# Performance work log

Hardware: AMD Instinct MI355X
Metric: run time of the kernel (lower is better)

Reference implementation:

```python
import jax, jax.numpy as jnp
import numpy as np

D_MODEL = 512
H = 8
DH = D_MODEL // H
P = H * (H - 1) // 2  # 28 head pairs
THRESH = 0.1
B, N = 2, 2048

# pair indices (i<j) in the same row-major order as the nested torch loop
_I_IDX, _J_IDX = np.triu_indices(H, k=1)
I_IDX = jnp.asarray(_I_IDX)
J_IDX = jnp.asarray(_J_IDX)


def setup_inputs() -> dict:
    key = jax.random.key(0)
    ks = jax.random.split(key, 10)
    s = 1.0 / np.sqrt(D_MODEL)
    return {
        "x": jax.random.normal(ks[0], (B, N, D_MODEL), dtype=jnp.float32),
        "Wq": jax.random.normal(ks[1], (D_MODEL, D_MODEL), dtype=jnp.float32) * s,
        "bq": jnp.zeros((D_MODEL,), dtype=jnp.float32),
        "Wk": jax.random.normal(ks[2], (D_MODEL, D_MODEL), dtype=jnp.float32) * s,
        "bk": jnp.zeros((D_MODEL,), dtype=jnp.float32),
        "Wv": jax.random.normal(ks[3], (D_MODEL, D_MODEL), dtype=jnp.float32) * s,
        "bv": jnp.zeros((D_MODEL,), dtype=jnp.float32),
        "Wo": jax.random.normal(ks[4], (D_MODEL, D_MODEL), dtype=jnp.float32) * s,
        "bo": jnp.zeros((D_MODEL,), dtype=jnp.float32),
        # stacked restriction maps: (P, DH_out, DH_in), Linear(bias=False)
        "Wr": jax.random.normal(ks[5], (P, DH, DH), dtype=jnp.float32) / np.sqrt(DH),
        "agreement_scale": jnp.asarray(1.0, dtype=jnp.float32),
    }


def reference(x, Wq, bq, Wk, bk, Wv, bv, Wo, bo, Wr, agreement_scale):
    b, n, d = x.shape
    # projections (torch Linear: y = x @ W.T + b), split into heads -> (B,H,N,DH)
    q = (x @ Wq.T + bq).reshape(b, n, H, DH).transpose(0, 2, 1, 3)
    k = (x @ Wk.T + bk).reshape(b, n, H, DH).transpose(0, 2, 1, 3)
    v = (x @ Wv.T + bv).reshape(b, n, H, DH).transpose(0, 2, 1, 3)

    scores = jnp.einsum("bhnd,bhmd->bhnm", q, k) / jnp.sqrt(jnp.asarray(DH, x.dtype))
    attn = jax.nn.softmax(scores, axis=-1)
    head_out = jnp.einsum("bhnm,bhmd->bhnd", attn, v)  # (B,H,N,DH)

    # --- pairwise restriction-map agreement, fully batched over the P pairs ---
    hi = head_out[:, I_IDX]  # (B,P,N,DH)
    hj = head_out[:, J_IDX]  # (B,P,N,DH)
    ri = jnp.einsum("bpnd,ped->bpne", hi, Wr)  # per-pair Linear(bias=False)
    diff = jnp.linalg.norm(ri - hj, axis=-1).mean(axis=-1)  # (B,P)
    score = jnp.exp(-diff * agreement_scale / THRESH)  # (B,P)

    agreement = jnp.zeros((b, H, H), dtype=x.dtype)
    agreement = agreement.at[:, I_IDX, J_IDX].set(score)
    agreement = agreement.at[:, J_IDX, I_IDX].set(score)
    diag = jnp.arange(H)
    agreement = agreement.at[:, diag, diag].set(1.0)

    # --- consensus aggregation ---
    offdiag = 1.0 - jnp.eye(H, dtype=x.dtype)
    consensus = (agreement * offdiag).sum(axis=-1) / (H - 1)  # (B,H)
    filtered = consensus * (consensus > THRESH).astype(x.dtype)
    weights = jax.nn.softmax(filtered + 1e-10, axis=-1)  # (B,H)

    agg = (head_out * weights[:, :, None, None]).sum(axis=1)  # (B,N,DH)
    agg = jnp.tile(agg, (1, 1, H))  # torch .repeat(1,1,H) -> (B,N,D)
    return agg @ Wo.T + bo
```

## Files before the change

### kernel.cpp

```cpp
#include <hip/hip_runtime.h>
#include <stdint.h>

typedef __attribute__((ext_vector_type(8))) short bf16x8;
typedef __attribute__((ext_vector_type(4))) float f32x4;
typedef __attribute__((ext_vector_type(4))) unsigned short u16x4;

#define LDS_SWZ(row, col) (((((col) >> 3) ^ ((row) & 7)) << 4))

__device__ __forceinline__ unsigned short f2bf(float f) {
  union { float f; unsigned u; } v; v.f = f;
  unsigned r = v.u + 0x7FFFu + ((v.u >> 16) & 1u);
  return (unsigned short)(r >> 16);
}
__device__ __forceinline__ float bf2f(unsigned short h) {
  union { unsigned u; float f; } v; v.u = ((unsigned)h) << 16;
  return v.f;
}
__device__ __forceinline__ void gld_lds16(const void* g, void* l) {
  __builtin_amdgcn_global_load_lds((const __attribute__((address_space(1))) void*)g,
                                   (__attribute__((address_space(3))) void*)l, 16, 0, 0);
}

__global__ void k_prep(const float* __restrict__ x, const float* __restrict__ wq,
                       const float* __restrict__ wk, const float* __restrict__ wv,
                       const float* __restrict__ wr, const float* __restrict__ wo,
                       unsigned short* __restrict__ xb, unsigned short* __restrict__ wb,
                       unsigned short* __restrict__ wrb, unsigned short* __restrict__ wsb) {
  int q = blockIdx.x * blockDim.x + threadIdx.x;
  if (q >= 749568) {
    int t = q - 749568;
    if (t >= 512 * 64) return;
    int e = t >> 6, d = t & 63;
    float s = 0.f;
#pragma unroll
    for (int qq = 0; qq < 8; ++qq) s += wo[e * 512 + qq * 64 + d];
    wsb[t] = f2bf(s);
    return;
  }
  const float* src; unsigned short* dst; int off;
  if (q < 524288)      { src = x;  dst = xb;          off = q; }
  else if (q < 589824) { src = wq; dst = wb;          off = q - 524288; }
  else if (q < 655360) { src = wk; dst = wb + 262144; off = q - 589824; }
  else if (q < 720896) { src = wv; dst = wb + 524288; off = q - 655360; }
  else                 { src = wr; dst = wrb;         off = q - 720896; }
  float4 v = ((const float4*)src)[off];
  u16x4 o; o.x = f2bf(v.x); o.y = f2bf(v.y); o.z = f2bf(v.z); o.w = f2bf(v.w);
  ((u16x4*)dst)[off] = o;
}

__global__ __launch_bounds__(256) void k_qkv(
    const unsigned short* __restrict__ xb, const unsigned short* __restrict__ wb,
    const float* __restrict__ bq, const float* __restrict__ bk, const float* __restrict__ bv,
    unsigned short* __restrict__ qb, unsigned short* __restrict__ kb,
    unsigned short* __restrict__ vtb) {
  __shared__ alignas(16) unsigned char As[2][128 * 128];
  __shared__ alignas(16) unsigned char Bs[2][64 * 128];
  const int tid = threadIdx.x;
  const int wave = tid >> 6, lane = tid & 63;
  const int rowbase = blockIdx.x * 128;
  const int colbase = blockIdx.y * 64;
  const int z = blockIdx.z;
  const unsigned short* W = wb + z * 512 * 512;
  const float* bias = (z == 0) ? bq : ((z == 1) ? bk : bv);
  f32x4 acc[2][4] = {};

#define QKV_STAGE(buf, kt_)                                                            \
  do {                                                                                 \
    _Pragma("unroll") for (int i_ = 0; i_ < 4; ++i_) {                                 \
      const int L_ = i_ * 256 + tid;                                                   \
      const int row_ = L_ >> 3, pos_ = L_ & 7;                                         \
      gld_lds16(xb + (rowbase + row_) * 512 + (kt_) * 64 + ((pos_ ^ (row_ & 7)) << 3), \
                As[buf] + (i_ * 256 + wave * 64) * 16);                                \
    }                                                                                  \
    _Pragma("unroll") for (int i_ = 0; i_ < 2; ++i_) {                                 \
      const int L_ = i_ * 256 + tid;                                                   \
      const int row_ = L_ >> 3, pos_ = L_ & 7;                                         \
      gld_lds16(W + (colbase + row_) * 512 + (kt_) * 64 + ((pos_ ^ (row_ & 7)) << 3),  \
                Bs[buf] + (i_ * 256 + wave * 64) * 16);                                \
    }                                                                                  \
  } while (0)

  QKV_STAGE(0, 0);
  __syncthreads();
  for (int kt = 0; kt < 8; ++kt) {
    const int cur = kt & 1;
    if (kt < 7) QKV_STAGE(cur ^ 1, kt + 1);
#pragma unroll
    for (int kc = 0; kc < 2; ++kc) {
      bf16x8 af[2], bfr[4];
#pragma unroll
      for (int mq = 0; mq < 2; ++mq) {
        const int row = wave * 32 + mq * 16 + (lane & 15);
        const int col = kc * 32 + ((lane >> 4) << 3);
        af[mq] = *(const bf16x8*)(As[cur] + row * 128 + LDS_SWZ(row, col));
      }
#pragma unroll
      for (int nq = 0; nq < 4; ++nq) {
        const int row = nq * 16 + (lane & 15);
        const int col = kc * 32 + ((lane >> 4) << 3);
        bfr[nq] = *(const bf16x8*)(Bs[cur] + row * 128 + LDS_SWZ(row, col));
      }
#pragma unroll
      for (int mq = 0; mq < 2; ++mq)
#pragma unroll
        for (int nq = 0; nq < 4; ++nq)
          acc[mq][nq] = __builtin_amdgcn_mfma_f32_16x16x32_bf16(af[mq], bfr[nq], acc[mq][nq], 0, 0, 0);
    }
    __syncthreads();
  }
  const float qs = 0.18033688011112043f;
#pragma unroll
  for (int mq = 0; mq < 2; ++mq)
#pragma unroll
    for (int nq = 0; nq < 4; ++nq)
#pragma unroll
      for (int r = 0; r < 4; ++r) {
        const int grow = rowbase + wave * 32 + mq * 16 + ((lane >> 4) << 2) + r;
        const int col = colbase + nq * 16 + (lane & 15);
        float v = acc[mq][nq][r] + bias[col];
        const int b = grow >> 11, n = grow & 2047;
        const int h = col >> 6, dh = col & 63;
        if (z == 0)      qb[(((b << 3) + h) * 2048 + n) * 64 + dh] = f2bf(v * qs);
        else if (z == 1) kb[(((b << 3) + h) * 2048 + n) * 64 + dh] = f2bf(v);
        else             vtb[((((b << 3) + h) << 6) + dh) * 2048 + n] = f2bf(v);
      }
}

__global__ __launch_bounds__(512, 4) void k_attn(
    const unsigned short* __restrict__ qb, const unsigned short* __restrict__ kb,
    const unsigned short* __restrict__ vtb, unsigned short* __restrict__ hob) {
  __shared__ alignas(16) unsigned char smem[81920];
  const int tid = threadIdx.x, wave = tid >> 6, lane = tid & 63;
  const int team = wave >> 2, w4 = wave & 3;
  const int ttid = tid & 255;
  const int bh = blockIdx.x >> 5;
  const int qt = blockIdx.x & 31;
  const int n0 = qt * 64 + w4 * 16;
  unsigned char* Kt = smem + team * 32768;
  unsigned char* Vt = Kt + 16384;
  unsigned char* pw = smem + 65536 + wave * 2048;
  const unsigned short* kbase = kb + bh * 2048 * 64;
  const unsigned short* vbase = vtb + bh * 64 * 2048;
  bf16x8 qf[2];
#pragma unroll
  for (int kc = 0; kc < 2; ++kc)
    qf[kc] = *(const bf16x8*)(qb + (bh * 2048 + n0 + (lane & 15)) * 64 + kc * 32 + ((lane >> 4) << 3));
  f32x4 oacc[4] = {};
  float mrun[4], lpart[4];
#pragma unroll
  for (int r = 0; r < 4; ++r) { mrun[r] = -1e30f; lpart[r] = 0.f; }

#define ATTN_STAGE(buf, T_)                                                        \
  do {                                                                             \
    _Pragma("unroll") for (int i_ = 0; i_ < 2; ++i_) {                             \
      const int L_ = i_ * 256 + ttid;                                              \
      const int row_ = L_ >> 3, pos_ = L_ & 7;                                     \
      gld_lds16(kbase + ((T_) * 64 + row_) * 64 + ((pos_ ^ (row_ & 7)) << 3),      \
                Kt + (buf) * 8192 + (i_ * 256 + w4 * 64) * 16);                    \
      gld_lds16(vbase + row_ * 2048 + (T_) * 64 + ((pos_ ^ (row_ & 7)) << 3),      \
                Vt + (buf) * 8192 + (i_ * 256 + w4 * 64) * 16);                    \
    }                                                                              \
  } while (0)

  ATTN_STAGE(0, team * 16);
  __syncthreads();
  for (int t = 0; t < 16; ++t) {
    const int cur = t & 1;
    if (t < 15) ATTN_STAGE(cur ^ 1, team * 16 + t + 1);
    f32x4 s[4];
#pragma unroll
    for (int mc = 0; mc < 4; ++mc) {
      f32x4 zz = {};
#pragma unroll
      for (int kc = 0; kc < 2; ++kc) {
        const int row = mc * 16 + (lane & 15);
        const int col = kc * 32 + ((lane >> 4) << 3);
        bf16x8 kf = *(const bf16x8*)(Kt + cur * 8192 + row * 128 + LDS_SWZ(row, col));
        zz = __builtin_amdgcn_mfma_f32_16x16x32_bf16(qf[kc], kf, zz, 0, 0, 0);
      }
      s[mc] = zz;
    }
    float lm[4];
#pragma unroll
    for (int r = 0; r < 4; ++r)
      lm[r] = fmaxf(fmaxf(s[0][r], s[1][r]), fmaxf(s[2][r], s[3][r]));
    bool need = (lm[0] > mrun[0] + 8.f) | (lm[1] > mrun[1] + 8.f) |
                (lm[2] > mrun[2] + 8.f) | (lm[3] > mrun[3] + 8.f);
    if (__any(need)) {
      float sc[4];
#pragma unroll
      for (int r = 0; r < 4; ++r) {
        float v = lm[r];
#pragma unroll
        for (int off = 1; off < 16; off <<= 1) v = fmaxf(v, __shfl_xor(v, off));
        float mnew = fmaxf(mrun[r], v);
        sc[r] = exp2f(mrun[r] - mnew);
        mrun[r] = mnew;
        lpart[r] *= sc[r];
      }
#pragma unroll
      for (int c2 = 0; c2 < 4; ++c2) {
        f32x4 o = oacc[c2];
#pragma unroll
        for (int r = 0; r < 4; ++r) o[r] *= sc[r];
        oacc[c2] = o;
      }
    }
    float pl[4][4];
#pragma unroll
    for (int r = 0; r < 4; ++r) {
      float ps = 0.f;
#pragma unroll
      for (int mc = 0; mc < 4; ++mc) { float p = exp2f(s[mc][r] - mrun[r]); pl[mc][r] = p; ps += p; }
      lpart[r] += ps;
    }
#pragma unroll
    for (int mc = 0; mc < 4; ++mc)
#pragma unroll
      for (int r = 0; r < 4; ++r) {
        const int row = ((lane >> 4) << 2) + r;
        const int col = mc * 16 + (lane & 15);
        *(unsigned short*)(pw + row * 128 + LDS_SWZ(row, col) + ((col & 7) << 1)) = f2bf(pl[mc][r]);
      }
    bf16x8 pa[2];
#pragma unroll
    for (int kc = 0; kc < 2; ++kc) {
      const int row = (lane & 15);
      const int col = kc * 32 + ((lane >> 4) << 3);
      pa[kc] = *(const bf16x8*)(pw + row * 128 + LDS_SWZ(row, col));
    }
#pragma unroll
    for (int c2 = 0; c2 < 4; ++c2) {
      f32x4 o = oacc[c2];
#pragma unroll
      for (int kc = 0; kc < 2; ++kc) {
        const int row = c2 * 16 + (lane & 15);
        const int col = kc * 32 + ((lane >> 4) << 3);
        bf16x8 vf = *(const bf16x8*)(Vt + cur * 8192 + row * 128 + LDS_SWZ(row, col));
        o = __builtin_amdgcn_mfma_f32_16x16x32_bf16(pa[kc], vf, o, 0, 0, 0);
      }
      oacc[c2] = o;
    }
    __syncthreads();
  }
  float lsum[4];
#pragma unroll
  for (int r = 0; r < 4; ++r) {
    float v = lpart[r];
#pragma unroll
    for (int off = 1; off < 16; off <<= 1) v += __shfl_xor(v, off);
    lsum[r] = v;
  }
  float* ex = (float*)smem;
  float* p = ex + (w4 * 64 + lane) * 24;
  if (team == 1) {
#pragma unroll
    for (int c2 = 0; c2 < 4; ++c2)
#pragma unroll
      for (int r = 0; r < 4; ++r) p[c2 * 4 + r] = oacc[c2][r];
#pragma unroll
    for (int r = 0; r < 4; ++r) { p[16 + r] = mrun[r]; p[20 + r] = lsum[r]; }
  }
  __syncthreads();
  if (team == 0) {
    float m1[4], l1[4], w0[4], w1[4];
#pragma unroll
    for (int r = 0; r < 4; ++r) {
      m1[r] = p[16 + r]; l1[r] = p[20 + r];
      float ms = fmaxf(mrun[r], m1[r]);
      float a = exp2f(mrun[r] - ms), bq_ = exp2f(m1[r] - ms);
      float li = 1.f / (a * lsum[r] + bq_ * l1[r]);
      w0[r] = a * li; w1[r] = bq_ * li;
    }
#pragma unroll
    for (int c2 = 0; c2 < 4; ++c2)
#pragma unroll
      for (int r = 0; r < 4; ++r) {
        const int n = n0 + ((lane >> 4) << 2) + r;
        const int dh = c2 * 16 + (lane & 15);
        float o1 = p[c2 * 4 + r];
        hob[(bh * 2048 + n) * 64 + dh] = f2bf(w0[r] * oacc[c2][r] + w1[r] * o1);
      }
  }
}

__global__ __launch_bounds__(256) void k_pair(const unsigned short* __restrict__ hob,
                                              const unsigned short* __restrict__ wrb,
                                              float* __restrict__ dpart) {
  __shared__ alignas(16) unsigned char Ws[64 * 128];
  __shared__ alignas(16) unsigned char Hj[2][64 * 128];
  __shared__ float red[4];
  const int tid = threadIdx.x, wave = tid >> 6, lane = tid & 63;
  const int chunk = blockIdx.x & 7, bp = blockIdx.x >> 3;
  const int b = bp / 28, p = bp % 28;
  int pp = p, ii = 0;
  while (pp >= 7 - ii) { pp -= 7 - ii; ii++; }
  const int i = ii, j = ii + 1 + pp;
  const unsigned short* hib = hob + ((b * 8 + i) * 2048) * 64;
  const unsigned short* hjb = hob + ((b * 8 + j) * 2048) * 64;

#define PAIR_STAGE(buf, t_)                                                      \
  do {                                                                           \
    _Pragma("unroll") for (int is_ = 0; is_ < 2; ++is_) {                        \
      const int L_ = is_ * 256 + tid;                                            \
      const int row_ = L_ >> 3, pos_ = L_ & 7;                                   \
      gld_lds16(hjb + ((t_) * 64 + row_) * 64 + ((pos_ ^ (row_ & 7)) << 3),      \
                Hj[buf] + (is_ * 256 + wave * 64) * 16);                         \
    }                                                                            \
  } while (0)

#pragma unroll
  for (int is = 0; is < 2; ++is) {
    const int L = is * 256 + tid;
    const int row = L >> 3, pos = L & 7;
    gld_lds16(wrb + (p * 64 + row) * 64 + ((pos ^ (row & 7)) << 3), Ws + (is * 256 + wave * 64) * 16);
  }
  PAIR_STAGE(0, chunk * 4);
  __syncthreads();
  bf16x8 wf[4][2];
#pragma unroll
  for (int c = 0; c < 4; ++c)
#pragma unroll
    for (int kc = 0; kc < 2; ++kc) {
      const int row = c * 16 + (lane & 15);
      const int col = kc * 32 + ((lane >> 4) << 3);
      wf[c][kc] = *(const bf16x8*)(Ws + row * 128 + LDS_SWZ(row, col));
    }
  float wacc = 0.f;
  for (int t = 0; t < 4; ++t) {
    const int tt = chunk * 4 + t;
    const int cur = t & 1;
    if (t < 3) PAIR_STAGE(cur ^ 1, tt + 1);
    const int rbase = tt * 64 + wave * 16;
    f32x4 ri[4] = {};
#pragma unroll
    for (int kc = 0; kc < 2; ++kc) {
      bf16x8 hf = *(const bf16x8*)(hib + (rbase + (lane & 15)) * 64 + kc * 32 + ((lane >> 4) << 3));
#pragma unroll
      for (int c = 0; c < 4; ++c)
        ri[c] = __builtin_amdgcn_mfma_f32_16x16x32_bf16(hf, wf[c][kc], ri[c], 0, 0, 0);
    }
#pragma unroll
    for (int r = 0; r < 4; ++r) {
      const int row = wave * 16 + ((lane >> 4) << 2) + r;
      float ss = 0.f;
#pragma unroll
      for (int c = 0; c < 4; ++c) {
        const int col = c * 16 + (lane & 15);
        float hv = bf2f(*(const unsigned short*)(Hj[cur] + (row & 63) * 128 + LDS_SWZ(row & 63, col) + ((col & 7) << 1)));
        float d = ri[c][r] - hv;
        ss += d * d;
      }
#pragma unroll
      for (int off = 1; off < 16; off <<= 1) ss += __shfl_xor(ss, off);
      if ((lane & 15) == 0) wacc += sqrtf(ss);
    }
    __syncthreads();
  }
  float tot = __shfl(wacc, 0) + __shfl(wacc, 16) + __shfl(wacc, 32) + __shfl(wacc, 48);
  if (lane == 0) red[wave] = tot;
  __syncthreads();
  if (tid == 0) dpart[blockIdx.x] = red[0] + red[1] + red[2] + red[3];
}

__global__ __launch_bounds__(256) void k_agg(const unsigned short* __restrict__ hob,
                                             const float* __restrict__ dpart,
                                             const float* __restrict__ scal,
                                             unsigned short* __restrict__ aggb) {
  __shared__ float sc_s[2][28];
  __shared__ float filt[2][8];
  __shared__ float wts_s[16];
  const int tid = threadIdx.x;
  if (tid < 56) {
    int bb = tid / 28, pp = tid % 28;
    int base = (bb * 28 + pp) * 8;
    float diff = 0.f;
#pragma unroll
    for (int c = 0; c < 8; ++c) diff += dpart[base + c];
    diff /= 2048.f;
    sc_s[bb][pp] = expf(-diff * scal[0] / 0.1f);
  }
  __syncthreads();
  if (tid < 16) {
    int bb = tid / 8, h = tid % 8;
    float cons = 0.f;
    for (int h2 = 0; h2 < 8; ++h2)
      if (h2 != h) {
        int i_ = h < h2 ? h : h2, j_ = h < h2 ? h2 : h;
        int pp = i_ * (15 - i_) / 2 + (j_ - i_ - 1);
        cons += sc_s[bb][pp];
      }
    cons /= 7.f;
    filt[bb][h] = (cons > 0.1f) ? cons : 0.f;
  }
  __syncthreads();
  if (tid < 16) {
    int bb = tid / 8, h = tid % 8;
    float m = -1e30f;
    for (int h2 = 0; h2 < 8; ++h2) m = fmaxf(m, filt[bb][h2] + 1e-10f);
    float s = 0.f;
    for (int h2 = 0; h2 < 8; ++h2) s += expf(filt[bb][h2] + 1e-10f - m);
    wts_s[tid] = expf(filt[bb][h] + 1e-10f - m) / s;
  }
  __syncthreads();
  int t = blockIdx.x * blockDim.x + tid;
  if (t >= 4096 * 8) return;
  int r = t >> 3, dblk = t & 7;
  int b = r >> 11, n = r & 2047;
  float acc[8] = {};
#pragma unroll
  for (int h = 0; h < 8; ++h) {
    float w = wts_s[b * 8 + h];
    bf16x8 v = *(const bf16x8*)(hob + (((b * 8 + h) << 11) + n) * 64 + dblk * 8);
#pragma unroll
    for (int e = 0; e < 8; ++e) acc[e] += w * bf2f((unsigned short)v[e]);
  }
  bf16x8 o;
#pragma unroll
  for (int e = 0; e < 8; ++e) o[e] = (short)f2bf(acc[e]);
  *(bf16x8*)(aggb + r * 64 + dblk * 8) = o;
}

__global__ __launch_bounds__(256) void k_out(const unsigned short* __restrict__ aggb,
                                             const unsigned short* __restrict__ wsb,
                                             const float* __restrict__ bo,
                                             float* __restrict__ out) {
  __shared__ alignas(16) unsigned char Ws[64 * 128];
  const int tid = threadIdx.x, wave = tid >> 6, lane = tid & 63;
  const int rowb = blockIdx.x * 64, colb = blockIdx.y * 64;
#pragma unroll
  for (int is = 0; is < 2; ++is) {
    const int L = is * 256 + tid;
    const int row = L >> 3, pos = L & 7;
    gld_lds16(wsb + (colb + row) * 64 + ((pos ^ (row & 7)) << 3), Ws + (is * 256 + wave * 64) * 16);
  }
  __syncthreads();
  bf16x8 af[2];
#pragma unroll
  for (int kc = 0; kc < 2; ++kc)
    af[kc] = *(const bf16x8*)(aggb + (rowb + wave * 16 + (lane & 15)) * 64 + kc * 32 + ((lane >> 4) << 3));
  f32x4 acc[4] = {};
#pragma unroll
  for (int c = 0; c < 4; ++c)
#pragma unroll
    for (int kc = 0; kc < 2; ++kc) {
      const int row = c * 16 + (lane & 15);
      const int col = kc * 32 + ((lane >> 4) << 3);
      bf16x8 wfr = *(const bf16x8*)(Ws + row * 128 + LDS_SWZ(row, col));
      acc[c] = __builtin_amdgcn_mfma_f32_16x16x32_bf16(af[kc], wfr, acc[c], 0, 0, 0);
    }
#pragma unroll
  for (int c = 0; c < 4; ++c)
#pragma unroll
    for (int r = 0; r < 4; ++r) {
      const int grow = rowb + wave * 16 + ((lane >> 4) << 2) + r;
      const int col = colb + c * 16 + (lane & 15);
      out[grow * 512 + col] = acc[c][r] + bo[col];
    }
}

extern "C" void kernel_launch(void* const* d_in, const int* in_sizes, int n_in,
                              void* d_out, int out_size, void* d_ws, size_t ws_size,
                              hipStream_t stream) {
  const float* x  = (const float*)d_in[0];
  const float* Wq = (const float*)d_in[1];
  const float* bq = (const float*)d_in[2];
  const float* Wk = (const float*)d_in[3];
  const float* bk = (const float*)d_in[4];
  const float* Wv = (const float*)d_in[5];
  const float* bv = (const float*)d_in[6];
  const float* Wo = (const float*)d_in[7];
  const float* bo = (const float*)d_in[8];
  const float* Wr = (const float*)d_in[9];
  const float* ascale = (const float*)d_in[10];
  float* out = (float*)d_out;

  char* ws = (char*)d_ws;
  unsigned short* xb   = (unsigned short*)(ws);
  unsigned short* qb   = (unsigned short*)(ws + (4u << 20));
  unsigned short* kb   = (unsigned short*)(ws + (8u << 20));
  unsigned short* vtb  = (unsigned short*)(ws + (12u << 20));
  unsigned short* hob  = (unsigned short*)(ws + (16u << 20));
  unsigned short* wb   = (unsigned short*)(ws + (20u << 20));
  unsigned short* wrb  = (unsigned short*)(ws + (20u << 20) + 3u * 512 * 512 * 2);
  unsigned short* wsb  = (unsigned short*)(ws + (20u << 20) + 3u * 512 * 512 * 2 + 28u * 64 * 64 * 2);
  unsigned short* aggb = (unsigned short*)(ws + (22u << 20));
  float* dpart = (float*)(ws + (23u << 20));

  k_prep<<<3056, 256, 0, stream>>>(x, Wq, Wk, Wv, Wr, Wo, xb, wb, wrb, wsb);
  k_qkv<<<dim3(32, 8, 3), 256, 0, stream>>>(xb, wb, bq, bk, bv, qb, kb, vtb);
  k_attn<<<512, 512, 0, stream>>>(qb, kb, vtb, hob);
  k_pair<<<448, 256, 0, stream>>>(hob, wrb, dpart);
  k_agg<<<128, 256, 0, stream>>>(hob, dpart, ascale, aggb);
  k_out<<<dim3(64, 8), 256, 0, stream>>>(aggb, wsb, bo, out);
}
```

Measured before the change: 83.03 us.

## Transpose QK^T MFMA so each lane owns one query row in attention

Swaps the MFMA operands for the score tile so that S^T is produced and each lane holds all four values for a single query row. The per-row max and sum collapse to a scalar per lane, which removes the 16-lane shuffle reductions and replaces them with two xor shuffles over the lane groups. P is packed two bf16 at a time and written as a uint2 store instead of sixteen scalar short stores. The rescale factors and the final m/l statistics are redistributed with __shfl to match the output accumulator layout, and the exchange-buffer stride is padded to 25 floats to reduce bank conflicts. This adds per-iteration shuffles on the rescale path and depends on the transposed fragment layout being mapped correctly.

Result: faster. 78.78 us (-5.1%).

```diff
diff --git a/kernel.cpp b/kernel.cpp
--- a/kernel.cpp
+++ b/kernel.cpp
@@ -1,4 +1,5 @@
 #include <hip/hip_runtime.h>
+#include <hip/hip_bf16.h>
 #include <stdint.h>
 
 typedef __attribute__((ext_vector_type(8))) short bf16x8;
@@ -15,6 +16,10 @@
 __device__ __forceinline__ float bf2f(unsigned short h) {
   union { unsigned u; float f; } v; v.u = ((unsigned)h) << 16;
   return v.f;
+}
+__device__ __forceinline__ unsigned pk2bf(float a, float b) {
+  __hip_bfloat162 h2 = __float22bfloat162_rn(float2{a, b});
+  unsigned u; __builtin_memcpy(&u, &h2, 4); return u;
 }
 __device__ __forceinline__ void gld_lds16(const void* g, void* l) {
   __builtin_amdgcn_global_load_lds((const __attribute__((address_space(1))) void*)g,
@@ -136,6 +141,7 @@
   const int bh = blockIdx.x >> 5;
   const int qt = blockIdx.x & 31;
   const int n0 = qt * 64 + w4 * 16;
+  const int lq = lane & 15, lg = lane >> 4;
   unsigned char* Kt = smem + team * 32768;
   unsigned char* Vt = Kt + 16384;
   unsigned char* pw = smem + 65536 + wave * 2048;
@@ -144,11 +150,9 @@
   bf16x8 qf[2];
 #pragma unroll
   for (int kc = 0; kc < 2; ++kc)
-    qf[kc] = *(const bf16x8*)(qb + (bh * 2048 + n0 + (lane & 15)) * 64 + kc * 32 + ((lane >> 4) << 3));
+    qf[kc] = *(const bf16x8*)(qb + (bh * 2048 + n0 + lq) * 64 + kc * 32 + (lg << 3));
   f32x4 oacc[4] = {};
-  float mrun[4], lpart[4];
-#pragma unroll
-  for (int r = 0; r < 4; ++r) { mrun[r] = -1e30f; lpart[r] = 0.f; }
+  float mrun = -1e30f, lpart = 0.f;
 
 #define ATTN_STAGE(buf, T_)                                                        \
   do {                                                                             \
@@ -173,69 +177,57 @@
       f32x4 zz = {};
 #pragma unroll
       for (int kc = 0; kc < 2; ++kc) {
-        const int row = mc * 16 + (lane & 15);
-        const int col = kc * 32 + ((lane >> 4) << 3);
+        const int row = mc * 16 + lq;
+        const int col = kc * 32 + (lg << 3);
         bf16x8 kf = *(const bf16x8*)(Kt + cur * 8192 + row * 128 + LDS_SWZ(row, col));
-        zz = __builtin_amdgcn_mfma_f32_16x16x32_bf16(qf[kc], kf, zz, 0, 0, 0);
+        zz = __builtin_amdgcn_mfma_f32_16x16x32_bf16(kf, qf[kc], zz, 0, 0, 0);
       }
       s[mc] = zz;
     }
-    float lm[4];
-#pragma unroll
-    for (int r = 0; r < 4; ++r)
-      lm[r] = fmaxf(fmaxf(s[0][r], s[1][r]), fmaxf(s[2][r], s[3][r]));
-    bool need = (lm[0] > mrun[0] + 8.f) | (lm[1] > mrun[1] + 8.f) |
-                (lm[2] > mrun[2] + 8.f) | (lm[3] > mrun[3] + 8.f);
-    if (__any(need)) {
-      float sc[4];
-#pragma unroll
-      for (int r = 0; r < 4; ++r) {
-        float v = lm[r];
-#pragma unroll
-        for (int off = 1; off < 16; off <<= 1) v = fmaxf(v, __shfl_xor(v, off));
-        float mnew = fmaxf(mrun[r], v);
-        sc[r] = exp2f(mrun[r] - mnew);
-        mrun[r] = mnew;
-        lpart[r] *= sc[r];
-      }
+    float lm = s[0][0];
+#pragma unroll
+    for (int mc = 0; mc < 4; ++mc)
+#pragma unroll
+      for (int r = 0; r < 4; ++r) lm = fmaxf(lm, s[mc][r]);
+    if (__any(lm > mrun + 8.f)) {
+      float v = fmaxf(lm, __shfl_xor(lm, 16));
+      v = fmaxf(v, __shfl_xor(v, 32));
+      float mnew = fmaxf(mrun, v);
+      float sc = exp2f(mrun - mnew);
+      mrun = mnew; lpart *= sc;
+      float sco[4];
+#pragma unroll
+      for (int r = 0; r < 4; ++r) sco[r] = __shfl(sc, (lane & 48) | ((lg << 2) + r));
 #pragma unroll
       for (int c2 = 0; c2 < 4; ++c2) {
         f32x4 o = oacc[c2];
 #pragma unroll
-        for (int r = 0; r < 4; ++r) o[r] *= sc[r];
+        for (int r = 0; r < 4; ++r) o[r] *= sco[r];
         oacc[c2] = o;
       }
     }
     float pl[4][4];
 #pragma unroll
-    for (int r = 0; r < 4; ++r) {
+    for (int mc = 0; mc < 4; ++mc) {
       float ps = 0.f;
 #pragma unroll
-      for (int mc = 0; mc < 4; ++mc) { float p = exp2f(s[mc][r] - mrun[r]); pl[mc][r] = p; ps += p; }
-      lpart[r] += ps;
-    }
-#pragma unroll
-    for (int mc = 0; mc < 4; ++mc)
-#pragma unroll
-      for (int r = 0; r < 4; ++r) {
-        const int row = ((lane >> 4) << 2) + r;
-        const int col = mc * 16 + (lane & 15);
-        *(unsigned short*)(pw + row * 128 + LDS_SWZ(row, col) + ((col & 7) << 1)) = f2bf(pl[mc][r]);
-      }
+      for (int r = 0; r < 4; ++r) { float p = exp2f(s[mc][r] - mrun); pl[mc][r] = p; ps += p; }
+      lpart += ps;
+      const int kk = mc * 16 + (lg << 2);
+      uint2 pkd = { pk2bf(pl[mc][0], pl[mc][1]), pk2bf(pl[mc][2], pl[mc][3]) };
+      *(uint2*)(pw + lq * 128 + LDS_SWZ(lq, kk) + ((kk & 7) << 1)) = pkd;
+    }
     bf16x8 pa[2];
 #pragma unroll
-    for (int kc = 0; kc < 2; ++kc) {
-      const int row = (lane & 15);
-      const int col = kc * 32 + ((lane >> 4) << 3);
-      pa[kc] = *(const bf16x8*)(pw + row * 128 + LDS_SWZ(row, col));
-    }
+    for (int kc = 0; kc < 2; ++kc)
+      pa[kc] = *(const bf16x8*)(pw + lq * 128 + LDS_SWZ(lq, kc * 32 + (lg << 3)));
 #pragma unroll
     for (int c2 = 0; c2 < 4; ++c2) {
       f32x4 o = oacc[c2];
 #pragma unroll
       for (int kc = 0; kc < 2; ++kc) {
-        const int row = c2 * 16 + (lane & 15);
-        const int col = kc * 32 + ((lane >> 4) << 3);
+        const int row = c2 * 16 + lq;
+        const int col = kc * 32 + (lg << 3);
         bf16x8 vf = *(const bf16x8*)(Vt + cur * 8192 + row * 128 + LDS_SWZ(row, col));
         o = __builtin_amdgcn_mfma_f32_16x16x32_bf16(pa[kc], vf, o, 0, 0, 0);
       }
@@ -243,42 +235,43 @@
     }
     __syncthreads();
   }
-  float lsum[4];
+  float ltot = lpart + __shfl_xor(lpart, 16);
+  ltot += __shfl_xor(ltot, 32);
+  float m_o[4], l_o[4];
 #pragma unroll
   for (int r = 0; r < 4; ++r) {
-    float v = lpart[r];
-#pragma unroll
-    for (int off = 1; off < 16; off <<= 1) v += __shfl_xor(v, off);
-    lsum[r] = v;
+    const int src = (lane & 48) | ((lg << 2) + r);
+    m_o[r] = __shfl(mrun, src);
+    l_o[r] = __shfl(ltot, src);
   }
   float* ex = (float*)smem;
-  float* p = ex + (w4 * 64 + lane) * 24;
+  float* px = ex + (w4 * 64 + lane) * 25;
   if (team == 1) {
 #pragma unroll
     for (int c2 = 0; c2 < 4; ++c2)
 #pragma unroll
-      for (int r = 0; r < 4; ++r) p[c2 * 4 + r] = oacc[c2][r];
-#pragma unroll
-    for (int r = 0; r < 4; ++r) { p[16 + r] = mrun[r]; p[20 + r] = lsum[r]; }
+      for (int r = 0; r < 4; ++r) px[c2 * 4 + r] = oacc[c2][r];
+#pragma unroll
+    for (int r = 0; r < 4; ++r) { px[16 + r] = m_o[r]; px[20 + r] = l_o[r]; }
   }
   __syncthreads();
   if (team == 0) {
-    float m1[4], l1[4], w0[4], w1[4];
+    float w0[4], w1[4];
 #pragma unroll
     for (int r = 0; r < 4; ++r) {
-      m1[r] = p[16 + r]; l1[r] = p[20 + r];
-      float ms = fmaxf(mrun[r], m1[r]);
-      float a = exp2f(mrun[r] - ms), bq_ = exp2f(m1[r] - ms);
-      float li = 1.f / (a * lsum[r] + bq_ * l1[r]);
-      w0[r] = a * li; w1[r] = bq_ * li;
+      float m1 = px[16 + r], l1 = px[20 + r];
+      float ms = fmaxf(m_o[r], m1);
+      float a = exp2f(m_o[r] - ms), b = exp2f(m1 - ms);
+      float li = 1.f / (a * l_o[r] + b * l1);
+      w0[r] = a * li; w1[r] = b * li;
     }
 #pragma unroll
     for (int c2 = 0; c2 < 4; ++c2)
 #pragma unroll
       for (int r = 0; r < 4; ++r) {
-        const int n = n0 + ((lane >> 4) << 2) + r;
-        const int dh = c2 * 16 + (lane & 15);
-        float o1 = p[c2 * 4 + r];
+        const int n = n0 + (lg << 2) + r;
+        const int dh = c2 * 16 + lq;
+        float o1 = px[c2 * 4 + r];
         hob[(bh * 2048 + n) * 64 + dh] = f2bf(w0[r] * oacc[c2][r] + w1[r] * o1);
       }
   }
```
